# Optimization experiments

Hardware: AMD Instinct MI355X
Metric: run time of the kernel (lower is better)

## Reference

```python
import jax, jax.numpy as jnp
import numpy as np

C_S, C_P, FEAT_DIM, NUM_BINS = 256, 128, 64, 22
TOTAL_EDGE_FEATS = FEAT_DIM * 3 + NUM_BINS * 2  # 236
MAX_LEN = 2056


def get_index_embedding(indices, embed_size, max_len=MAX_LEN):
    # indices: [..., ] float; returns [..., embed_size]
    K = jnp.arange(embed_size // 2, dtype=jnp.float32)
    ang = indices[..., None] * jnp.pi / (max_len ** (2.0 * K / embed_size))
    return jnp.concatenate([jnp.sin(ang), jnp.cos(ang)], axis=-1)


def calc_distogram(pos, min_bin, max_bin, num_bins):
    # pos: [B, N, 3] -> one-hot distogram [B, N, N, num_bins]
    d = jnp.linalg.norm(pos[:, :, None, :] - pos[:, None, :, :], axis=-1)[..., None]
    lower = jnp.linspace(min_bin, max_bin, num_bins)
    upper = jnp.concatenate([lower[1:], jnp.array([1e8], dtype=jnp.float32)])
    return ((d > lower) & (d < upper)).astype(pos.dtype)


def layer_norm(x, gamma, beta, eps=1e-5):
    mu = jnp.mean(x, axis=-1, keepdims=True)
    var = jnp.mean((x - mu) ** 2, axis=-1, keepdims=True)
    return (x - mu) * jax.lax.rsqrt(var + eps) * gamma + beta


def setup_inputs() -> dict:
    key = jax.random.key(0)
    ks = jax.random.split(key, 12)
    B, N = 2, 512
    def lin(k, fan_in, shape):
        bound = 1.0 / np.sqrt(fan_in)
        return jax.random.uniform(k, shape, jnp.float32, -bound, bound)
    return {
        "s": jax.random.normal(ks[0], (B, N, C_S), jnp.float32),
        "t": jax.random.normal(ks[1], (B, N, 3), jnp.float32),
        "sc_t": jax.random.normal(ks[2], (B, N, 3), jnp.float32),
        "p_mask": jnp.ones((B, N, N), jnp.float32),
        "W_sp": lin(ks[3], C_S, (FEAT_DIM, C_S)),
        "b_sp": lin(ks[4], C_S, (FEAT_DIM,)),
        "W_rp": lin(ks[5], FEAT_DIM, (FEAT_DIM, FEAT_DIM)),
        "b_rp": lin(ks[5], FEAT_DIM, (FEAT_DIM,)),
        "W1": lin(ks[6], TOTAL_EDGE_FEATS, (C_P, TOTAL_EDGE_FEATS)),
        "b1": lin(ks[7], TOTAL_EDGE_FEATS, (C_P,)),
        "W2": lin(ks[8], C_P, (C_P, C_P)),
        "b2": lin(ks[9], C_P, (C_P,)),
        "W3": lin(ks[10], C_P, (C_P, C_P)),
        "b3": lin(ks[11], C_P, (C_P,)),
        "ln_g": jnp.ones((C_P,), jnp.float32),
        "ln_b": jnp.zeros((C_P,), jnp.float32),
    }


def reference(s, t, sc_t, p_mask, W_sp, b_sp, W_rp, b_rp, W1, b1, W2, b2, W3, b3, ln_g, ln_b):
    B, N, _ = s.shape
    # node embed then all-pairs broadcast-concat: [B,N,N,2*feat_dim]
    p_i = s @ W_sp.T + b_sp  # [B,N,feat_dim]
    cross = jnp.concatenate([
        jnp.broadcast_to(p_i[:, :, None, :], (B, N, N, FEAT_DIM)),
        jnp.broadcast_to(p_i[:, None, :, :], (B, N, N, FEAT_DIM)),
    ], axis=-1)
    # relative position embedding (res_idx=None -> arange)
    pos = jnp.broadcast_to(jnp.arange(N, dtype=jnp.float32)[None, :], (B, N))
    rel_pos = pos[:, :, None] - pos[:, None, :]
    pos_emb = get_index_embedding(rel_pos, FEAT_DIM)  # [B,N,N,feat_dim]
    relpos_feats = pos_emb @ W_rp.T + b_rp
    dist_feats = calc_distogram(t, 1e-3, 20.0, NUM_BINS)
    sc_feats = calc_distogram(sc_t, 1e-3, 20.0, NUM_BINS)
    all_edge = jnp.concatenate([cross, relpos_feats, dist_feats, sc_feats], axis=-1)
    h = jax.nn.relu(all_edge @ W1.T + b1)
    h = jax.nn.relu(h @ W2.T + b2)
    h = h @ W3.T + b3
    h = layer_norm(h, ln_g, ln_b)
    return h * p_mask[..., None]
```

## Files before the change

kernel.cpp:

```cpp
#include <hip/hip_runtime.h>

#define NN 512

typedef __attribute__((ext_vector_type(8))) short bf16x8;
typedef __attribute__((ext_vector_type(4))) float f32x4;

__device__ __forceinline__ unsigned short f2bf(float x) {
    union { float f; unsigned u; } c; c.f = x;
    unsigned u = c.u + 0x7fffu + ((c.u >> 16) & 1u);
    return (unsigned short)(u >> 16);
}

__device__ __forceinline__ float blo(unsigned u) {
    union { unsigned x; float f; } c; c.x = u << 16; return c.f;
}
__device__ __forceinline__ float bhi(unsigned u) {
    union { unsigned x; float f; } c; c.x = u & 0xffff0000u; return c.f;
}

__device__ __forceinline__ unsigned pk2(unsigned a, unsigned b, unsigned c,
                                        unsigned d, unsigned e) {
    float lo = blo(a) + blo(b) + blo(c) + blo(d) + blo(e);
    float hi = bhi(a) + bhi(b) + bhi(c) + bhi(d) + bhi(e);
    lo = fmaxf(lo, 0.0f);
    hi = fmaxf(hi, 0.0f);
    return (unsigned)f2bf(lo) | ((unsigned)f2bf(hi) << 16);
}

__device__ __forceinline__ int find_bin(float d) {
    const float stepf   = (float)((20.0 - 1e-3) / 21.0);
    const float invstep = (float)(21.0 / (20.0 - 1e-3));
    int kc = (int)floorf((d - 1e-3f) * invstep);
    int bin = 22;
    #pragma unroll
    for (int dk = -1; dk <= 1; ++dk) {
        int k = kc + dk;
        if (k >= 0 && k <= 21) {
            float lo = fmaf((float)k, stepf, 1e-3f);
            float hi = (k < 21) ? fmaf((float)(k + 1), stepf, 1e-3f) : 1e8f;
            if (d > lo && d < hi) bin = k;
        }
    }
    return bin;
}

__global__ __launch_bounds__(128) void k_prep(
        const float* __restrict__ s, const float* __restrict__ t,
        const float* __restrict__ sct,
        const float* __restrict__ Wsp, const float* __restrict__ bsp,
        const float* __restrict__ Wrp, const float* __restrict__ brp,
        const float* __restrict__ W1, const float* __restrict__ b1,
        const float* __restrict__ W2, const float* __restrict__ W3,
        float* __restrict__ p_i, unsigned short* __restrict__ relTb,
        unsigned short* __restrict__ WdTb, unsigned short* __restrict__ WscTb,
        unsigned short* __restrict__ w2a, unsigned short* __restrict__ w3a,
        unsigned short* __restrict__ binT)
{
    __shared__ float sh[2][256];
    const int blk = blockIdx.x, tid = threadIdx.x;

    if (blk < 23) {
        const int bin = blk, c = tid;
        WdTb[bin * 128 + c]  = (bin < 22) ? f2bf(W1[c * 236 + 192 + bin]) : (unsigned short)0;
        WscTb[bin * 128 + c] = (bin < 22) ? f2bf(W1[c * 236 + 214 + bin]) : (unsigned short)0;
    } else if (blk < 55) {
        const int seg = blk - 23;
        const int isW3 = seg >> 4;
        const int idx = (seg & 15) * 128 + tid;
        const int lane = idx & 63, ks = (idx >> 6) & 3, ct = idx >> 8;
        const float* W = isW3 ? W3 : W2;
        unsigned short* dst = isW3 ? w3a : w2a;
        const float* wp = W + (ct * 16 + (lane & 15)) * 128 + ks * 32 + (lane >> 4) * 8;
        unsigned r0 = (unsigned)f2bf(wp[0]) | ((unsigned)f2bf(wp[1]) << 16);
        unsigned r1 = (unsigned)f2bf(wp[2]) | ((unsigned)f2bf(wp[3]) << 16);
        unsigned r2 = (unsigned)f2bf(wp[4]) | ((unsigned)f2bf(wp[5]) << 16);
        unsigned r3 = (unsigned)f2bf(wp[6]) | ((unsigned)f2bf(wp[7]) << 16);
        uint4 v = { r0, r1, r2, r3 };
        *(uint4*)(dst + idx * 8) = v;
    } else if (blk < 1078) {
        const int row = blk - 55;
        const float d = (float)(row - 511);
        if (tid < 32) {
            float f = powf(2056.0f, (float)tid * (1.0f / 32.0f));
            float ang = d * 3.14159265358979323846f / f;
            sh[0][tid] = sinf(ang);
            sh[0][tid + 32] = cosf(ang);
        }
        __syncthreads();
        if (tid < 64) {
            const float* wr = Wrp + tid * 64;
            float a = brp[tid];
            #pragma unroll
            for (int k = 0; k < 64; ++k) a += sh[0][k] * wr[k];
            sh[1][tid] = a;
        }
        __syncthreads();
        const float* w = W1 + tid * 236 + 128;
        float a = b1[tid];
        #pragma unroll
        for (int k = 0; k < 64; ++k) a += sh[1][k] * w[k];
        relTb[row * 128 + tid] = f2bf(a);
    } else if (blk < 1590) {
        const int half = tid >> 6, ch = tid & 63;
        const int row = (blk - 1078) * 2 + half;
        *(float4*)&sh[half][ch * 4] = *(const float4*)&s[row * 256 + ch * 4];
        __syncthreads();
        const float* w = Wsp + ch * 256;
        float acc = bsp[ch];
        #pragma unroll 8
        for (int k = 0; k < 256; k += 4)
            acc += sh[half][k]*w[k] + sh[half][k+1]*w[k+1] + sh[half][k+2]*w[k+2] + sh[half][k+3]*w[k+3];
        p_i[row * 64 + ch] = acc;
    } else {
        const int pair = (blk - 1590) * 128 + tid;
        const int bi = pair >> 9, j = pair & (NN - 1);
        const int rj = (bi & ~(NN - 1)) + j;
        float ax = t[bi*3+0] - t[rj*3+0];
        float ay = t[bi*3+1] - t[rj*3+1];
        float az = t[bi*3+2] - t[rj*3+2];
        int bD = find_bin(sqrtf(ax*ax + ay*ay + az*az));
        float sx = sct[bi*3+0] - sct[rj*3+0];
        float sy = sct[bi*3+1] - sct[rj*3+1];
        float sz = sct[bi*3+2] - sct[rj*3+2];
        int bS = find_bin(sqrtf(sx*sx + sy*sy + sz*sz));
        binT[pair] = (unsigned short)(bD | (bS << 5));
    }
}

__global__ __launch_bounds__(128) void k_ql(const float* __restrict__ p_i,
        const float* __restrict__ W1,
        unsigned short* __restrict__ qLb, unsigned short* __restrict__ qRb)
{
    __shared__ float pr[64];
    const int row = blockIdx.x, tid = threadIdx.x;
    if (tid < 16) *(float4*)&pr[tid * 4] = *(const float4*)&p_i[row * 64 + tid * 4];
    __syncthreads();
    const float* w = W1 + tid * 236;
    float aL = 0.f, aR = 0.f;
    #pragma unroll
    for (int k = 0; k < 64; ++k) { aL += pr[k] * w[k]; aR += pr[k] * w[64 + k]; }
    qLb[row * 128 + tid] = f2bf(aL);
    qRb[row * 128 + tid] = f2bf(aR);
}

#define H1_OFF  0
#define H2_OFF  16384
#define LNP_OFF 32768
#define SMEM_SZ 35840

__global__ __launch_bounds__(512, 4) void k_main(
    const float* __restrict__ pmask,
    const unsigned short* __restrict__ qLb, const unsigned short* __restrict__ qRb,
    const unsigned short* __restrict__ relTb, const unsigned short* __restrict__ WdTb,
    const unsigned short* __restrict__ WscTb, const unsigned short* __restrict__ binT,
    const unsigned short* __restrict__ w2a, const unsigned short* __restrict__ w3a,
    const float* __restrict__ b2, const float* __restrict__ b3,
    const float* __restrict__ lng, const float* __restrict__ lnb,
    float* __restrict__ out)
{
    __shared__ __align__(16) char smem[SMEM_SZ];

    const int tid  = threadIdx.x;
    const int l    = tid & 63;
    const int w    = tid >> 6;
    const int wr   = w >> 2;
    const int wc   = w & 3;
    const int jloc = l & 15;
    const int gq   = l >> 4;

    const int blk   = (blockIdx.x & 7) * 1024 + (blockIdx.x >> 3);
    const int bi    = blk >> 3;
    const int i     = bi & (NN - 1);
    const int bbase = bi & ~(NN - 1);
    const int j0    = (blk & 7) * 64;

    bf16x8 w2r[2][4], w3r[2][4];
    #pragma unroll
    for (int cc = 0; cc < 2; ++cc)
        #pragma unroll
        for (int ks = 0; ks < 4; ++ks) {
            const int fi = ((wc * 2 + cc) * 256 + ks * 64 + l) * 8;
            w2r[cc][ks] = *(const bf16x8*)(w2a + fi);
            w3r[cc][ks] = *(const bf16x8*)(w3a + fi);
        }
    float maskv[2];
    #pragma unroll
    for (int rt = 0; rt < 2; ++rt)
        maskv[rt] = pmask[(size_t)bi * NN + j0 + wr * 32 + rt * 16 + jloc];

    {
        const int r = tid >> 3, q = tid & 7;
        const unsigned bv = binT[bi * NN + j0 + r];
        const int bD = bv & 31, bS = (int)(bv >> 5);
        const unsigned short* qLp = qLb + (size_t)bi * 128;
        const unsigned short* qRp = qRb + (size_t)(bbase + j0 + r) * 128;
        const unsigned short* rTp = relTb + (size_t)(i - (j0 + r) + NN - 1) * 128;
        const unsigned short* dTp = WdTb + bD * 128;
        const unsigned short* sTp = WscTb + bS * 128;
        const int hswz = (r & 7) << 4;
        #pragma unroll
        for (int u = 0; u < 2; ++u) {
            const int c0 = q * 16 + u * 8;
            uint4 A = *(const uint4*)(qLp + c0);
            uint4 B = *(const uint4*)(qRp + c0);
            uint4 C = *(const uint4*)(rTp + c0);
            uint4 D = *(const uint4*)(dTp + c0);
            uint4 E = *(const uint4*)(sTp + c0);
            uint4 P;
            P.x = pk2(A.x, B.x, C.x, D.x, E.x);
            P.y = pk2(A.y, B.y, C.y, D.y, E.y);
            P.z = pk2(A.z, B.z, C.z, D.z, E.z);
            P.w = pk2(A.w, B.w, C.w, D.w, E.w);
            *(uint4*)(smem + H1_OFF + ((r * 256 + c0 * 2) ^ hswz)) = P;
        }
    }
    __syncthreads();

    const int rswz = (jloc & 7) << 4;

    #pragma unroll
    for (int rt = 0; rt < 2; ++rt) {
        const int rowb = (wr * 32 + rt * 16 + jloc) * 256;
        f32x4 a2[2] = { {0.f,0.f,0.f,0.f}, {0.f,0.f,0.f,0.f} };
        #pragma unroll
        for (int ks = 0; ks < 4; ++ks) {
            bf16x8 bfr = *(bf16x8*)(smem + H1_OFF + ((rowb + ks * 64 + gq * 16) ^ rswz));
            a2[0] = __builtin_amdgcn_mfma_f32_16x16x32_bf16(w2r[0][ks], bfr, a2[0], 0, 0, 0);
            a2[1] = __builtin_amdgcn_mfma_f32_16x16x32_bf16(w2r[1][ks], bfr, a2[1], 0, 0, 0);
        }
        #pragma unroll
        for (int cc = 0; cc < 2; ++cc) {
            const int c = wc * 32 + cc * 16 + gq * 4;
            float4 bb = *(const float4*)(b2 + c);
            float y0 = fmaxf(a2[cc][0] + bb.x, 0.0f);
            float y1 = fmaxf(a2[cc][1] + bb.y, 0.0f);
            float y2 = fmaxf(a2[cc][2] + bb.z, 0.0f);
            float y3 = fmaxf(a2[cc][3] + bb.w, 0.0f);
            uint2 pk;
            pk.x = (unsigned)f2bf(y0) | ((unsigned)f2bf(y1) << 16);
            pk.y = (unsigned)f2bf(y2) | ((unsigned)f2bf(y3) << 16);
            *(uint2*)(smem + H2_OFF + ((rowb + c * 2) ^ rswz)) = pk;
        }
    }
    __syncthreads();

    f32x4 acc3[2][2];
    float* lnp = (float*)(smem + LNP_OFF);
    #pragma unroll
    for (int rt = 0; rt < 2; ++rt) {
        const int rowb = (wr * 32 + rt * 16 + jloc) * 256;
        f32x4 a3[2] = { {0.f,0.f,0.f,0.f}, {0.f,0.f,0.f,0.f} };
        #pragma unroll
        for (int ks = 0; ks < 4; ++ks) {
            bf16x8 bfr = *(bf16x8*)(smem + H2_OFF + ((rowb + ks * 64 + gq * 16) ^ rswz));
            a3[0] = __builtin_amdgcn_mfma_f32_16x16x32_bf16(w3r[0][ks], bfr, a3[0], 0, 0, 0);
            a3[1] = __builtin_amdgcn_mfma_f32_16x16x32_bf16(w3r[1][ks], bfr, a3[1], 0, 0, 0);
        }
        float s1 = 0.f, s2 = 0.f;
        #pragma unroll
        for (int cc = 0; cc < 2; ++cc) {
            const int c = wc * 32 + cc * 16 + gq * 4;
            float4 bb = *(const float4*)(b3 + c);
            a3[cc][0] += bb.x; a3[cc][1] += bb.y;
            a3[cc][2] += bb.z; a3[cc][3] += bb.w;
            acc3[cc][rt] = a3[cc];
            #pragma unroll
            for (int r = 0; r < 4; ++r) { float v = a3[cc][r]; s1 += v; s2 += v * v; }
        }
        s1 += __shfl_xor(s1, 16); s2 += __shfl_xor(s2, 16);
        s1 += __shfl_xor(s1, 32); s2 += __shfl_xor(s2, 32);
        if (l < 16) {
            const int row = wr * 32 + rt * 16 + jloc;
            *(float2*)(lnp + row * 12 + wc * 2) = make_float2(s1, s2);
        }
    }
    __syncthreads();

    #pragma unroll
    for (int rt = 0; rt < 2; ++rt) {
        const int row = wr * 32 + rt * 16 + jloc;
        float4 v0 = *(float4*)(lnp + row * 12);
        float4 v1 = *(float4*)(lnp + row * 12 + 4);
        const float s1 = v0.x + v0.z + v1.x + v1.z;
        const float s2 = v0.y + v0.w + v1.y + v1.w;
        const float mean = s1 * (1.0f / 128.0f);
        const float var  = s2 * (1.0f / 128.0f) - mean * mean;
        const float rstd = rsqrtf(var + 1e-5f);
        const float mk = maskv[rt];
        #pragma unroll
        for (int cc = 0; cc < 2; ++cc) {
            const int c = wc * 32 + cc * 16 + gq * 4;
            float4 g4  = *(const float4*)(lng + c);
            float4 be4 = *(const float4*)(lnb + c);
            f32x4 a3 = acc3[cc][rt];
            f32x4 o;
            o[0] = ((a3[0] - mean) * rstd * g4.x + be4.x) * mk;
            o[1] = ((a3[1] - mean) * rstd * g4.y + be4.y) * mk;
            o[2] = ((a3[2] - mean) * rstd * g4.z + be4.z) * mk;
            o[3] = ((a3[3] - mean) * rstd * g4.w + be4.w) * mk;
            const int slot = (wc * 8 + cc * 4 + gq) ^ (row & 31);
            *(f32x4*)(smem + row * 512 + slot * 16) = o;
        }
    }
    __syncthreads();

    float* ob = out + ((size_t)(bi * NN + j0)) * 128;
    #pragma unroll
    for (int it = 0; it < 4; ++it) {
        const int boff = it * 8192 + tid * 16;
        const int row  = boff >> 9;
        const int slot = (boff >> 4) & 31;
        const int sslt = slot ^ (row & 31);
        f32x4 v = *(f32x4*)(smem + row * 512 + sslt * 16);
        __builtin_nontemporal_store(v, (f32x4*)(ob + (boff >> 2)));
    }
}

extern "C" void kernel_launch(void* const* d_in, const int* in_sizes, int n_in,
                              void* d_out, int out_size, void* d_ws, size_t ws_size,
                              hipStream_t stream)
{
    const float* s   = (const float*)d_in[0];
    const float* t   = (const float*)d_in[1];
    const float* sct = (const float*)d_in[2];
    const float* pm  = (const float*)d_in[3];
    const float* Wsp = (const float*)d_in[4];
    const float* bsp = (const float*)d_in[5];
    const float* Wrp = (const float*)d_in[6];
    const float* brp = (const float*)d_in[7];
    const float* W1  = (const float*)d_in[8];
    const float* b1  = (const float*)d_in[9];
    const float* W2  = (const float*)d_in[10];
    const float* b2  = (const float*)d_in[11];
    const float* W3  = (const float*)d_in[12];
    const float* b3  = (const float*)d_in[13];
    const float* lng = (const float*)d_in[14];
    const float* lnb = (const float*)d_in[15];

    float* ws = (float*)d_ws;
    float*          p_i   = ws;
    unsigned short* qLb   = (unsigned short*)(ws + 65536);
    unsigned short* qRb   = (unsigned short*)(ws + 131072);
    unsigned short* relTb = (unsigned short*)(ws + 196608);
    unsigned short* WdTb  = (unsigned short*)(ws + 262144);
    unsigned short* WscTb = (unsigned short*)(ws + 263616);
    unsigned short* w2a   = (unsigned short*)(ws + 265088);
    unsigned short* w3a   = (unsigned short*)(ws + 273280);
    unsigned short* binT  = (unsigned short*)(ws + 281472);

    k_prep<<<5686, 128, 0, stream>>>(s, t, sct, Wsp, bsp, Wrp, brp, W1, b1, W2, W3,
                                     p_i, relTb, WdTb, WscTb, w2a, w3a, binT);
    k_ql<<<1024, 128, 0, stream>>>(p_i, W1, qLb, qRb);
    k_main<<<8192, 512, 0, stream>>>(pm, qLb, qRb, relTb, WdTb, WscTb, binT,
                                     w2a, w3a, b2, b3, lng, lnb, (float*)d_out);
}
```

Baseline: 128.5 us.

## Fuse q projection into prep kernel and compute distogram bins inline in main

Merges the separate k_ql launch into k_prep, so each node block computes p_i in shared memory and then its qL/qR projections, and drops the p_i global buffer. The pairwise distance-bin table (binT) is removed, and k_main now computes both bins directly from t and sc_t for each pair. This removes one kernel launch, the 4096 prep blocks that filled binT, and the binT reads and writes. In exchange k_main does a little more ALU work per row and reads t and sc_t.

```diff
diff --git a/kernel.cpp b/kernel.cpp
--- a/kernel.cpp
+++ b/kernel.cpp
@@ -45,18 +45,18 @@
 }
 
 __global__ __launch_bounds__(128) void k_prep(
-        const float* __restrict__ s, const float* __restrict__ t,
-        const float* __restrict__ sct,
+        const float* __restrict__ s,
         const float* __restrict__ Wsp, const float* __restrict__ bsp,
         const float* __restrict__ Wrp, const float* __restrict__ brp,
         const float* __restrict__ W1, const float* __restrict__ b1,
         const float* __restrict__ W2, const float* __restrict__ W3,
-        float* __restrict__ p_i, unsigned short* __restrict__ relTb,
+        unsigned short* __restrict__ relTb,
         unsigned short* __restrict__ WdTb, unsigned short* __restrict__ WscTb,
         unsigned short* __restrict__ w2a, unsigned short* __restrict__ w3a,
-        unsigned short* __restrict__ binT)
+        unsigned short* __restrict__ qLb, unsigned short* __restrict__ qRb)
 {
     __shared__ float sh[2][256];
+    __shared__ float pr[2][64];
     const int blk = blockIdx.x, tid = threadIdx.x;
 
     if (blk < 23) {
@@ -100,47 +100,30 @@
         #pragma unroll
         for (int k = 0; k < 64; ++k) a += sh[1][k] * w[k];
         relTb[row * 128 + tid] = f2bf(a);
-    } else if (blk < 1590) {
+    } else {
         const int half = tid >> 6, ch = tid & 63;
-        const int row = (blk - 1078) * 2 + half;
-        *(float4*)&sh[half][ch * 4] = *(const float4*)&s[row * 256 + ch * 4];
+        const int row0 = (blk - 1078) * 2;
+        *(float4*)&sh[half][ch * 4] = *(const float4*)&s[(row0 + half) * 256 + ch * 4];
         __syncthreads();
-        const float* w = Wsp + ch * 256;
-        float acc = bsp[ch];
-        #pragma unroll 8
-        for (int k = 0; k < 256; k += 4)
-            acc += sh[half][k]*w[k] + sh[half][k+1]*w[k+1] + sh[half][k+2]*w[k+2] + sh[half][k+3]*w[k+3];
-        p_i[row * 64 + ch] = acc;
-    } else {
-        const int pair = (blk - 1590) * 128 + tid;
-        const int bi = pair >> 9, j = pair & (NN - 1);
-        const int rj = (bi & ~(NN - 1)) + j;
-        float ax = t[bi*3+0] - t[rj*3+0];
-        float ay = t[bi*3+1] - t[rj*3+1];
-        float az = t[bi*3+2] - t[rj*3+2];
-        int bD = find_bin(sqrtf(ax*ax + ay*ay + az*az));
-        float sx = sct[bi*3+0] - sct[rj*3+0];
-        float sy = sct[bi*3+1] - sct[rj*3+1];
-        float sz = sct[bi*3+2] - sct[rj*3+2];
-        int bS = find_bin(sqrtf(sx*sx + sy*sy + sz*sz));
-        binT[pair] = (unsigned short)(bD | (bS << 5));
-    }
-}
-
-__global__ __launch_bounds__(128) void k_ql(const float* __restrict__ p_i,
-        const float* __restrict__ W1,
-        unsigned short* __restrict__ qLb, unsigned short* __restrict__ qRb)
-{
-    __shared__ float pr[64];
-    const int row = blockIdx.x, tid = threadIdx.x;
-    if (tid < 16) *(float4*)&pr[tid * 4] = *(const float4*)&p_i[row * 64 + tid * 4];
-    __syncthreads();
-    const float* w = W1 + tid * 236;
-    float aL = 0.f, aR = 0.f;
-    #pragma unroll
-    for (int k = 0; k < 64; ++k) { aL += pr[k] * w[k]; aR += pr[k] * w[64 + k]; }
-    qLb[row * 128 + tid] = f2bf(aL);
-    qRb[row * 128 + tid] = f2bf(aR);
+        {
+            const float* w = Wsp + ch * 256;
+            float acc = bsp[ch];
+            #pragma unroll 8
+            for (int k = 0; k < 256; k += 4)
+                acc += sh[half][k]*w[k] + sh[half][k+1]*w[k+1] + sh[half][k+2]*w[k+2] + sh[half][k+3]*w[k+3];
+            pr[half][ch] = acc;
+        }
+        __syncthreads();
+        const float* w = W1 + tid * 236;
+        #pragma unroll
+        for (int rr = 0; rr < 2; ++rr) {
+            float aL = 0.f, aR = 0.f;
+            #pragma unroll
+            for (int k = 0; k < 64; ++k) { aL += pr[rr][k] * w[k]; aR += pr[rr][k] * w[64 + k]; }
+            qLb[(row0 + rr) * 128 + tid] = f2bf(aL);
+            qRb[(row0 + rr) * 128 + tid] = f2bf(aR);
+        }
+    }
 }
 
 #define H1_OFF  0
@@ -150,9 +133,10 @@
 
 __global__ __launch_bounds__(512, 4) void k_main(
     const float* __restrict__ pmask,
+    const float* __restrict__ t, const float* __restrict__ sct,
     const unsigned short* __restrict__ qLb, const unsigned short* __restrict__ qRb,
     const unsigned short* __restrict__ relTb, const unsigned short* __restrict__ WdTb,
-    const unsigned short* __restrict__ WscTb, const unsigned short* __restrict__ binT,
+    const unsigned short* __restrict__ WscTb,
     const unsigned short* __restrict__ w2a, const unsigned short* __restrict__ w3a,
     const float* __restrict__ b2, const float* __restrict__ b3,
     const float* __restrict__ lng, const float* __restrict__ lnb,
@@ -190,10 +174,18 @@
 
     {
         const int r = tid >> 3, q = tid & 7;
-        const unsigned bv = binT[bi * NN + j0 + r];
-        const int bD = bv & 31, bS = (int)(bv >> 5);
+        const int gj = bbase + j0 + r;
+        float ax = t[bi*3+0] - t[gj*3+0];
+        float ay = t[bi*3+1] - t[gj*3+1];
+        float az = t[bi*3+2] - t[gj*3+2];
+        const int bD = find_bin(sqrtf(ax*ax + ay*ay + az*az));
+        float sx = sct[bi*3+0] - sct[gj*3+0];
+        float sy = sct[bi*3+1] - sct[gj*3+1];
+        float sz = sct[bi*3+2] - sct[gj*3+2];
+        const int bS = find_bin(sqrtf(sx*sx + sy*sy + sz*sz));
+
         const unsigned short* qLp = qLb + (size_t)bi * 128;
-        const unsigned short* qRp = qRb + (size_t)(bbase + j0 + r) * 128;
+        const unsigned short* qRp = qRb + (size_t)gj * 128;
         const unsigned short* rTp = relTb + (size_t)(i - (j0 + r) + NN - 1) * 128;
         const unsigned short* dTp = WdTb + bD * 128;
         const unsigned short* sTp = WscTb + bS * 128;
@@ -338,19 +330,16 @@
     const float* lnb = (const float*)d_in[15];
 
     float* ws = (float*)d_ws;
-    float*          p_i   = ws;
-    unsigned short* qLb   = (unsigned short*)(ws + 65536);
-    unsigned short* qRb   = (unsigned short*)(ws + 131072);
-    unsigned short* relTb = (unsigned short*)(ws + 196608);
-    unsigned short* WdTb  = (unsigned short*)(ws + 262144);
-    unsigned short* WscTb = (unsigned short*)(ws + 263616);
-    unsigned short* w2a   = (unsigned short*)(ws + 265088);
-    unsigned short* w3a   = (unsigned short*)(ws + 273280);
-    unsigned short* binT  = (unsigned short*)(ws + 281472);
-
-    k_prep<<<5686, 128, 0, stream>>>(s, t, sct, Wsp, bsp, Wrp, brp, W1, b1, W2, W3,
-                                     p_i, relTb, WdTb, WscTb, w2a, w3a, binT);
-    k_ql<<<1024, 128, 0, stream>>>(p_i, W1, qLb, qRb);
-    k_main<<<8192, 512, 0, stream>>>(pm, qLb, qRb, relTb, WdTb, WscTb, binT,
+    unsigned short* qLb   = (unsigned short*)ws;
+    unsigned short* qRb   = (unsigned short*)(ws + 65536);
+    unsigned short* relTb = (unsigned short*)(ws + 131072);
+    unsigned short* WdTb  = (unsigned short*)(ws + 196608);
+    unsigned short* WscTb = (unsigned short*)(ws + 198080);
+    unsigned short* w2a   = (unsigned short*)(ws + 199552);
+    unsigned short* w3a   = (unsigned short*)(ws + 207744);
+
+    k_prep<<<1590, 128, 0, stream>>>(s, Wsp, bsp, Wrp, brp, W1, b1, W2, W3,
+                                     relTb, WdTb, WscTb, w2a, w3a, qLb, qRb);
+    k_main<<<8192, 512, 0, stream>>>(pm, t, sct, qLb, qRb, relTb, WdTb, WscTb,
                                      w2a, w3a, b2, b3, lng, lnb, (float*)d_out);
 }
```

After: 151.1 us. 1.18x slower.
